# Kernel tuning notes

Hardware: AMD Instinct MI355X
Metric: run time of the kernel (lower is better)

Reference implementation:

```python
import jax, jax.numpy as jnp
import numpy as np

N, E, F_IN, F_OUT = 16384, 4096, 128, 128
EPS = 1e-6


def setup_inputs() -> dict:
    key = jax.random.key(0)
    k1, k2, k3 = jax.random.split(key, 3)
    H = (jax.random.uniform(k1, (N, E)) < 0.05).astype(jnp.float32)
    x = jax.random.normal(k2, (N, F_IN), dtype=jnp.float32)
    W = jax.random.normal(k3, (F_IN, F_OUT), dtype=jnp.float32) * 0.05
    return {"x": x, "H": H, "W": W}


def reference(x, H, W):
    # D_v^{-1} H D_e^{-1} H^T x W, computed without materializing the NxN
    # adjacency: diagonal matmuls become row/col broadcast scaling, and the
    # GEMM chain is reordered right-to-left (same math, associativity).
    d_e_inv = 1.0 / (H.sum(axis=0) + EPS)   # [E]
    d_v_inv = 1.0 / (H.sum(axis=1) + EPS)   # [N]
    xw = x @ W                               # [N, F_out]
    edge_msg = H.T @ xw                      # [E, F_out] gather onto edges
    edge_msg = d_e_inv[:, None] * edge_msg   # D_e^{-1}
    node_msg = H @ edge_msg                  # [N, F_out] scatter back to nodes
    return d_v_inv[:, None] * node_msg       # D_v^{-1}
```

## Files before the change

kernel.cpp:

```cpp
#include <hip/hip_runtime.h>
#include <stdint.h>

#define N_NODES 16384
#define N_EDGES 4096
#define FDIM    128
#define EPSF    1e-6f

typedef __attribute__((ext_vector_type(8))) short short8;
typedef __attribute__((ext_vector_type(4))) float f32x4;
typedef unsigned long long ull;

__device__ __forceinline__ unsigned short f2bf(float f) {
    uint32_t u = __float_as_uint(f);
    return (unsigned short)((u + 0x7FFFu + ((u >> 16) & 1u)) >> 16);
}
__device__ __forceinline__ short8 as_s8(uint4 v) {
    union { uint4 a; short8 b; } u; u.a = v; return u.b;
}

__device__ __forceinline__ short8 expand8(uint32_t half, int bitoff) {
    uint32_t b8 = (half >> bitoff) & 0xFFu;
    uint32_t lo = ((b8 & 0xFu) * 0x00204081u) & 0x01010101u;
    uint32_t hi = ((b8 >> 4) * 0x00204081u) & 0x01010101u;
    union { short8 v; uint32_t u[4]; } a;
#if __has_builtin(__builtin_amdgcn_perm)
    a.u[0] = __builtin_amdgcn_perm(0u, lo, 0x04010400u) * 0x3F80u;
    a.u[1] = __builtin_amdgcn_perm(0u, lo, 0x04030402u) * 0x3F80u;
    a.u[2] = __builtin_amdgcn_perm(0u, hi, 0x04010400u) * 0x3F80u;
    a.u[3] = __builtin_amdgcn_perm(0u, hi, 0x04030402u) * 0x3F80u;
#else
    a.u[0] = ((lo & 1u)         | ((lo >> 8) & 1u) << 16) * 0x3F80u;
    a.u[1] = (((lo >> 16) & 1u) | ((lo >> 24) & 1u) << 16) * 0x3F80u;
    a.u[2] = ((hi & 1u)         | ((hi >> 8) & 1u) << 16) * 0x3F80u;
    a.u[3] = (((hi >> 16) & 1u) | ((hi >> 24) & 1u) << 16) * 0x3F80u;
#endif
    return a.v;
}

__device__ __forceinline__ ull bit_transpose64(ull q, int lane) {
    const ull M32 = 0xFFFFFFFF00000000ull, M16 = 0xFFFF0000FFFF0000ull,
              M8 = 0xFF00FF00FF00FF00ull, M4 = 0xF0F0F0F0F0F0F0F0ull,
              M2 = 0xCCCCCCCCCCCCCCCCull, M1 = 0xAAAAAAAAAAAAAAAAull;
#define TSTEP(d, Md) { ull tv = __shfl_xor(q, d, 64); \
    q = ((lane & d) == 0) ? ((q & ~Md) | ((tv << d) & Md)) \
                          : ((q & Md) | ((tv >> d) & ~Md)); }
    TSTEP(32, M32) TSTEP(16, M16) TSTEP(8, M8) TSTEP(4, M4) TSTEP(2, M2) TSTEP(1, M1)
#undef TSTEP
    return q;
}

__global__ __launch_bounds__(256) void k_bitpack(const float* __restrict__ H,
        ull* __restrict__ bitsNE, float* __restrict__ dvinv) {
    int w = threadIdx.x >> 6, lane = threadIdx.x & 63;
    int n = blockIdx.x * 4 + w;
    const float4* hr = (const float4*)(H + (size_t)n * N_EDGES);
    ull* out = bitsNE + (size_t)n * (N_EDGES / 64);
    int cnt = 0;
    for (int c4 = 0; c4 < N_EDGES / 256; ++c4) {
        float4 v = hr[c4 * 64 + lane];
        ull b0 = __ballot(v.x > 0.5f);
        ull b1 = __ballot(v.y > 0.5f);
        ull b2 = __ballot(v.z > 0.5f);
        ull b3 = __ballot(v.w > 0.5f);
        cnt += __popcll(b0) + __popcll(b1) + __popcll(b2) + __popcll(b3);
        if (lane == 0) {
            #pragma unroll
            for (int q = 0; q < 4; ++q) {
                ull wq = ((b0 >> (16 * q)) & 0xFFFFull)
                       | (((b1 >> (16 * q)) & 0xFFFFull) << 16)
                       | (((b2 >> (16 * q)) & 0xFFFFull) << 32)
                       | (((b3 >> (16 * q)) & 0xFFFFull) << 48);
                out[c4 * 4 + q] = wq;
            }
        }
    }
    if (lane == 0) dvinv[n] = 1.0f / ((float)cnt + EPSF);
}

__global__ __launch_bounds__(256) void k_transpose_bf(const ull* __restrict__ bitsNE,
        ull* __restrict__ bitsEN) {
    int w = threadIdx.x >> 6, lane = threadIdx.x & 63;
    int wid = blockIdx.x * 4 + w;
    int nt = wid >> 3, etg = wid & 7;
    int pl = 4 * (lane & 15) + (lane >> 4);
    const ull* src = bitsNE + (size_t)(nt * 64 + pl) * (N_EDGES / 64);
    #pragma unroll
    for (int i = 0; i < 8; ++i) {
        int et = etg * 8 + i;
        ull q = src[et];
        q = bit_transpose64(q, lane);
        bitsEN[(size_t)(et * 64 + pl) * (N_NODES / 64) + nt] = q;
    }
}

__global__ __launch_bounds__(256) void k_edeg(const ull* __restrict__ bitsEN,
        float* __restrict__ deinv) {
    int w = threadIdx.x >> 6, lane = threadIdx.x & 63;
    int e = blockIdx.x * 4 + w;
    const ull* r = bitsEN + (size_t)e * (N_NODES / 64);
    int s = __popcll(r[lane]) + __popcll(r[lane + 64]) + __popcll(r[lane + 128]) + __popcll(r[lane + 192]);
    for (int o = 32; o; o >>= 1) s += __shfl_xor(s, o);
    if (lane == 0) deinv[e] = 1.0f / ((float)s + EPSF);
}

__global__ __launch_bounds__(256) void k_xw(const float* __restrict__ x, const float* __restrict__ W,
        unsigned short* __restrict__ xwTp) {
    __shared__ __attribute__((aligned(16))) unsigned short ldsWT[128 * 136];
    __shared__ __attribute__((aligned(16))) unsigned short ldsT[128 * 72];
    int t = threadIdx.x, lane = t & 63, w = t >> 6;
    int r16 = lane & 15, klane = lane >> 4;
    for (int i = 0; i < 64; ++i) {
        int idx = i * 256 + t;
        int k = idx >> 7, f = idx & 127;
        ldsWT[f * 136 + k] = f2bf(W[idx]);
    }
    __syncthreads();
    int nbase = blockIdx.x * 64;
    int row = nbase + w * 16 + r16;
    const float4* xr4 = (const float4*)(x + (size_t)row * FDIM);
    f32x4 acc[8] = {};
    for (int kb = 0; kb < 128; kb += 32) {
        float4 u0 = xr4[(kb >> 2) + klane * 2];
        float4 u1 = xr4[(kb >> 2) + klane * 2 + 1];
        union { short8 v; unsigned short u[8]; } a;
        a.u[0] = f2bf(u0.x); a.u[1] = f2bf(u0.y); a.u[2] = f2bf(u0.z); a.u[3] = f2bf(u0.w);
        a.u[4] = f2bf(u1.x); a.u[5] = f2bf(u1.y); a.u[6] = f2bf(u1.z); a.u[7] = f2bf(u1.w);
        #pragma unroll
        for (int fb = 0; fb < 8; ++fb) {
            short8 b = *(const short8*)&ldsWT[(fb * 16 + r16) * 136 + kb + klane * 8];
            acc[fb] = __builtin_amdgcn_mfma_f32_16x16x32_bf16(a.v, b, acc[fb], 0, 0, 0);
        }
    }
    #pragma unroll
    for (int fb = 0; fb < 8; ++fb)
        #pragma unroll
        for (int r = 0; r < 4; ++r)
            ldsT[(fb * 16 + r16) * 72 + 16 * r + w * 4 + klane] = f2bf(acc[fb][r]);
    __syncthreads();
    int f = t >> 1, part = t & 1;
    #pragma unroll
    for (int j = 0; j < 4; ++j)
        *(uint4*)&xwTp[(size_t)f * N_NODES + nbase + part * 32 + j * 8] =
            *(const uint4*)&ldsT[f * 72 + part * 32 + j * 8];
}

#define LOADP(Q0, Q1, BUF, p) do { \
    Q0 = brow0[(p)]; Q1 = brow1[(p)]; \
    const unsigned short* _src = bcol + (size_t)(p) * 64; \
    _Pragma("unroll") \
    for (int _fb = 0; _fb < 4; ++_fb) { \
        BUF[_fb * 2]     = *(const uint4*)(_src + _fb * fbstride); \
        BUF[_fb * 2 + 1] = *(const uint4*)(_src + _fb * fbstride + 32); \
    } } while (0)

#define COMPUTEP(Q0, Q1, BUF) do { \
    _Pragma("unroll") \
    for (int _s2 = 0; _s2 < 2; ++_s2) { \
        uint32_t _h0 = (uint32_t)(_s2 == 0 ? (Q0) : ((Q0) >> 32)); \
        uint32_t _h1 = (uint32_t)(_s2 == 0 ? (Q1) : ((Q1) >> 32)); \
        short8 _a0 = expand8(_h0, bitoff); \
        short8 _a1 = expand8(_h1, bitoff); \
        _Pragma("unroll") \
        for (int _f = 0; _f < 4; ++_f) { \
            short8 _b = as_s8(BUF[_f * 2 + _s2]); \
            acc[0][_f] = __builtin_amdgcn_mfma_f32_16x16x32_bf16(_a0, _b, acc[0][_f], 0, 0, 0); \
            acc[1][_f] = __builtin_amdgcn_mfma_f32_16x16x32_bf16(_a1, _b, acc[1][_f], 0, 0, 0); \
        } } } while (0)

template<bool FINAL>
__global__ __launch_bounds__(256, 2) void k_gemm_gen(
        const ull* __restrict__ bits, int krows,
        const unsigned short* __restrict__ BT, int K,
        float* __restrict__ Cout, const float* __restrict__ rowScale,
        int M, int npairs) {
    int t = threadIdx.x, lane = t & 63, w = t >> 6;
    int r16 = lane & 15, klane = lane >> 4;
    int bitoff = klane * 8;
    int wm = w >> 1, wf = w & 1;
    int mbase = blockIdx.x * 64 + wm * 32;
    int kq0 = blockIdx.z * npairs;
    const ull* brow0 = bits + (size_t)(mbase + r16) * krows + kq0;
    const ull* brow1 = brow0 + (size_t)16 * krows;
    const unsigned short* bcol = BT + (size_t)(wf * 64 + r16) * K + (size_t)kq0 * 64 + klane * 8;
    const size_t fbstride = (size_t)16 * K;
    f32x4 acc[2][4] = {};
    ull qA0, qA1, qB0, qB1;
    uint4 bufA[8], bufB[8];
    LOADP(qA0, qA1, bufA, 0);
    for (int p = 0; p < npairs; p += 2) {
        LOADP(qB0, qB1, bufB, p + 1);
        COMPUTEP(qA0, qA1, bufA);
        if (p + 2 < npairs) LOADP(qA0, qA1, bufA, p + 2);
        COMPUTEP(qB0, qB1, bufB);
    }
    #pragma unroll
    for (int fr = 0; fr < 2; ++fr)
        #pragma unroll
        for (int fb = 0; fb < 4; ++fb)
            #pragma unroll
            for (int r = 0; r < 4; ++r) {
                int row = mbase + fr * 16 + klane * 4 + r;
                int col = wf * 64 + fb * 16 + r16;
                float v = acc[fr][fb][r];
                if (FINAL)
                    Cout[(size_t)row * FDIM + col] = rowScale[row] * v;
                else
                    Cout[(size_t)blockIdx.z * M * FDIM + (size_t)row * FDIM + col] = v;
            }
}

__global__ __launch_bounds__(256) void k_reduce_scale_T(const float* __restrict__ partials,
        const float* __restrict__ deinv, unsigned short* __restrict__ emTp, int S) {
    __shared__ float lds[64 * 129];
    int t = threadIdx.x;
    int e0 = blockIdx.x * 64;
    for (int i = 0; i < 32; ++i) {
        int idx = i * 256 + t;
        int e_l = idx >> 7, f = idx & 127;
        float s = 0.f;
        for (int z = 0; z < S; ++z)
            s += partials[(size_t)z * N_EDGES * FDIM + (size_t)(e0 + e_l) * FDIM + f];
        lds[e_l * 129 + f] = s * deinv[e0 + e_l];
    }
    __syncthreads();
    for (int i = 0; i < 32; ++i) {
        int idx = i * 256 + t;
        int f = idx >> 6, j = idx & 63;
        int pj = 4 * (j & 15) + (j >> 4);
        emTp[(size_t)f * N_EDGES + e0 + j] = f2bf(lds[pj * 129 + f]);
    }
}

__global__ __launch_bounds__(256) void k_finalN(const float* __restrict__ partN,
        const float* __restrict__ dvinv, float* __restrict__ out) {
    const float4* pa = (const float4*)partN;
    const float4* pb = (const float4*)(partN + (size_t)N_NODES * FDIM);
    float4* o4 = (float4*)out;
    int t = threadIdx.x;
    #pragma unroll
    for (int i = 0; i < 4; ++i) {
        int idx = blockIdx.x * 1024 + i * 256 + t;
        float4 a = pa[idx], b = pb[idx];
        float s = dvinv[idx >> 5];
        o4[idx] = make_float4((a.x + b.x) * s, (a.y + b.y) * s,
                              (a.z + b.z) * s, (a.w + b.w) * s);
    }
}

extern "C" void kernel_launch(void* const* d_in, const int* in_sizes, int n_in,
                              void* d_out, int out_size, void* d_ws, size_t ws_size,
                              hipStream_t stream) {
    const float* x = (const float*)d_in[0];
    const float* H = (const float*)d_in[1];
    const float* W = (const float*)d_in[2];
    float* out = (float*)d_out;
    char* ws = (char*)d_ws;

    ull* bitsNE = (ull*)(ws);
    ull* bitsEN = (ull*)(ws + (8u << 20));
    unsigned short* xwTp = (unsigned short*)(ws + (16u << 20));
    unsigned short* emTp = (unsigned short*)(ws + (20u << 20));
    float* dvinv = (float*)(ws + (21u << 20));
    float* deinv = (float*)(ws + (21u << 20) + 65536);
    float* partE = (float*)(ws + (22u << 20));
    float* partN = (float*)(ws + (38u << 20));

    int SE = 8;
    while (SE > 1 && (22u << 20) + (size_t)SE * N_EDGES * FDIM * 4 > ws_size) SE >>= 1;
    bool sn2 = ws_size >= ((38u << 20) + (size_t)2 * N_NODES * FDIM * 4);

    hipLaunchKernelGGL(k_bitpack, dim3(4096), dim3(256), 0, stream, H, bitsNE, dvinv);
    hipLaunchKernelGGL(k_transpose_bf, dim3(512), dim3(256), 0, stream, bitsNE, bitsEN);
    hipLaunchKernelGGL(k_edeg, dim3(1024), dim3(256), 0, stream, bitsEN, deinv);
    hipLaunchKernelGGL(k_xw, dim3(256), dim3(256), 0, stream, x, W, xwTp);
    hipLaunchKernelGGL((k_gemm_gen<false>), dim3(64, 1, SE), dim3(256), 0, stream,
                       bitsEN, N_NODES / 64, xwTp, N_NODES, partE, (const float*)nullptr,
                       N_EDGES, (N_NODES / 64) / SE);
    hipLaunchKernelGGL(k_reduce_scale_T, dim3(64), dim3(256), 0, stream, partE, deinv, emTp, SE);
    if (sn2) {
        hipLaunchKernelGGL((k_gemm_gen<false>), dim3(256, 1, 2), dim3(256), 0, stream,
                           bitsNE, N_EDGES / 64, emTp, N_EDGES, partN, (const float*)nullptr,
                           N_NODES, (N_EDGES / 64) / 2);
        hipLaunchKernelGGL(k_finalN, dim3(512), dim3(256), 0, stream, partN, dvinv, out);
    } else {
        hipLaunchKernelGGL((k_gemm_gen<true>), dim3(256, 1, 1), dim3(256), 0, stream,
                           bitsNE, N_EDGES / 64, emTp, N_EDGES, out, dvinv,
                           N_NODES, N_EDGES / 64);
    }
}
```

Baseline: 302.2 us.

## Fuse edge-degree count into transpose, repack bits per lane, drop split-K node GEMM

Bitpacking now has each lane read 64 contiguous floats and build one 64-bit word from exponent bits, replacing the per-wave ballot loop. The lane permutation used in the bit layout is removed. The separate edge-degree kernel is dropped: degrees are accumulated with atomics inside the transpose kernel, and the reciprocal is computed in the reduce kernel. The node-side GEMM goes from a 2-way split plus finalize kernel to a single launch that scales rows in its epilogue. The 2-blocks-per-CU launch bound on the GEMM is relaxed. Together these cut launches and intermediate traffic, at the cost of atomics and less parallelism in the final GEMM.

```diff
diff --git a/kernel.cpp b/kernel.cpp
--- a/kernel.cpp
+++ b/kernel.cpp
@@ -50,61 +50,61 @@
 }
 
 __global__ __launch_bounds__(256) void k_bitpack(const float* __restrict__ H,
-        ull* __restrict__ bitsNE, float* __restrict__ dvinv) {
-    int w = threadIdx.x >> 6, lane = threadIdx.x & 63;
-    int n = blockIdx.x * 4 + w;
-    const float4* hr = (const float4*)(H + (size_t)n * N_EDGES);
-    ull* out = bitsNE + (size_t)n * (N_EDGES / 64);
-    int cnt = 0;
-    for (int c4 = 0; c4 < N_EDGES / 256; ++c4) {
-        float4 v = hr[c4 * 64 + lane];
-        ull b0 = __ballot(v.x > 0.5f);
-        ull b1 = __ballot(v.y > 0.5f);
-        ull b2 = __ballot(v.z > 0.5f);
-        ull b3 = __ballot(v.w > 0.5f);
-        cnt += __popcll(b0) + __popcll(b1) + __popcll(b2) + __popcll(b3);
-        if (lane == 0) {
-            #pragma unroll
-            for (int q = 0; q < 4; ++q) {
-                ull wq = ((b0 >> (16 * q)) & 0xFFFFull)
-                       | (((b1 >> (16 * q)) & 0xFFFFull) << 16)
-                       | (((b2 >> (16 * q)) & 0xFFFFull) << 32)
-                       | (((b3 >> (16 * q)) & 0xFFFFull) << 48);
-                out[c4 * 4 + q] = wq;
-            }
+        ull* __restrict__ bitsNE, float* __restrict__ dvinv, int* __restrict__ ecnt) {
+    int t = threadIdx.x, w = t >> 6, lane = t & 63;
+    if (blockIdx.x == 0) {
+        int4 z = make_int4(0, 0, 0, 0);
+        #pragma unroll
+        for (int i = 0; i < 4; ++i) ((int4*)ecnt)[t * 4 + i] = z;
+    }
+    #pragma unroll
+    for (int r2 = 0; r2 < 2; ++r2) {
+        int n = blockIdx.x * 8 + w * 2 + r2;
+        const uint4* hr = (const uint4*)(H + (size_t)n * N_EDGES) + lane * 16;
+        uint32_t lo = 0, hi = 0;
+        #pragma unroll
+        for (int j = 0; j < 8; ++j) {
+            uint4 u = hr[j];
+            lo |= ((u.x >> 23) & 1u) << (4 * j);
+            lo |= ((u.y >> 23) & 1u) << (4 * j + 1);
+            lo |= ((u.z >> 23) & 1u) << (4 * j + 2);
+            lo |= ((u.w >> 23) & 1u) << (4 * j + 3);
         }
-    }
-    if (lane == 0) dvinv[n] = 1.0f / ((float)cnt + EPSF);
+        #pragma unroll
+        for (int j = 0; j < 8; ++j) {
+            uint4 u = hr[8 + j];
+            hi |= ((u.x >> 23) & 1u) << (4 * j);
+            hi |= ((u.y >> 23) & 1u) << (4 * j + 1);
+            hi |= ((u.z >> 23) & 1u) << (4 * j + 2);
+            hi |= ((u.w >> 23) & 1u) << (4 * j + 3);
+        }
+        ull q = (ull)lo | ((ull)hi << 32);
+        bitsNE[(size_t)n * (N_EDGES / 64) + lane] = q;
+        int cnt = __popcll(q);
+        #pragma unroll
+        for (int o = 32; o; o >>= 1) cnt += __shfl_xor(cnt, o);
+        if (lane == 0) dvinv[n] = 1.0f / ((float)cnt + EPSF);
+    }
 }
 
 __global__ __launch_bounds__(256) void k_transpose_bf(const ull* __restrict__ bitsNE,
-        ull* __restrict__ bitsEN) {
+        ull* __restrict__ bitsEN, int* __restrict__ ecnt) {
     int w = threadIdx.x >> 6, lane = threadIdx.x & 63;
     int wid = blockIdx.x * 4 + w;
     int nt = wid >> 3, etg = wid & 7;
-    int pl = 4 * (lane & 15) + (lane >> 4);
-    const ull* src = bitsNE + (size_t)(nt * 64 + pl) * (N_EDGES / 64);
+    const ull* src = bitsNE + (size_t)(nt * 64 + lane) * (N_EDGES / 64);
     #pragma unroll
     for (int i = 0; i < 8; ++i) {
         int et = etg * 8 + i;
         ull q = src[et];
         q = bit_transpose64(q, lane);
-        bitsEN[(size_t)(et * 64 + pl) * (N_NODES / 64) + nt] = q;
-    }
-}
-
-__global__ __launch_bounds__(256) void k_edeg(const ull* __restrict__ bitsEN,
-        float* __restrict__ deinv) {
-    int w = threadIdx.x >> 6, lane = threadIdx.x & 63;
-    int e = blockIdx.x * 4 + w;
-    const ull* r = bitsEN + (size_t)e * (N_NODES / 64);
-    int s = __popcll(r[lane]) + __popcll(r[lane + 64]) + __popcll(r[lane + 128]) + __popcll(r[lane + 192]);
-    for (int o = 32; o; o >>= 1) s += __shfl_xor(s, o);
-    if (lane == 0) deinv[e] = 1.0f / ((float)s + EPSF);
+        bitsEN[(size_t)(et * 64 + lane) * (N_NODES / 64) + nt] = q;
+        atomicAdd(&ecnt[et * 64 + lane], __popcll(q));
+    }
 }
 
 __global__ __launch_bounds__(256) void k_xw(const float* __restrict__ x, const float* __restrict__ W,
-        unsigned short* __restrict__ xwTp) {
+        unsigned short* __restrict__ xwT) {
     __shared__ __attribute__((aligned(16))) unsigned short ldsWT[128 * 136];
     __shared__ __attribute__((aligned(16))) unsigned short ldsT[128 * 72];
     int t = threadIdx.x, lane = t & 63, w = t >> 6;
@@ -135,12 +135,12 @@
     for (int fb = 0; fb < 8; ++fb)
         #pragma unroll
         for (int r = 0; r < 4; ++r)
-            ldsT[(fb * 16 + r16) * 72 + 16 * r + w * 4 + klane] = f2bf(acc[fb][r]);
+            ldsT[(fb * 16 + r16) * 72 + w * 16 + klane * 4 + r] = f2bf(acc[fb][r]);
     __syncthreads();
     int f = t >> 1, part = t & 1;
     #pragma unroll
     for (int j = 0; j < 4; ++j)
-        *(uint4*)&xwTp[(size_t)f * N_NODES + nbase + part * 32 + j * 8] =
+        *(uint4*)&xwT[(size_t)f * N_NODES + nbase + part * 32 + j * 8] =
             *(const uint4*)&ldsT[f * 72 + part * 32 + j * 8];
 }
 
@@ -168,7 +168,7 @@
         } } } while (0)
 
 template<bool FINAL>
-__global__ __launch_bounds__(256, 2) void k_gemm_gen(
+__global__ __launch_bounds__(256) void k_gemm_gen(
         const ull* __restrict__ bits, int krows,
         const unsigned short* __restrict__ BT, int K,
         float* __restrict__ Cout, const float* __restrict__ rowScale,
@@ -210,40 +210,25 @@
 }
 
 __global__ __launch_bounds__(256) void k_reduce_scale_T(const float* __restrict__ partials,
-        const float* __restrict__ deinv, unsigned short* __restrict__ emTp, int S) {
+        const int* __restrict__ ecnt, unsigned short* __restrict__ emT, int S) {
     __shared__ float lds[64 * 129];
+    __shared__ float sdeinv[64];
     int t = threadIdx.x;
     int e0 = blockIdx.x * 64;
+    if (t < 64) sdeinv[t] = 1.0f / ((float)ecnt[e0 + t] + EPSF);
     for (int i = 0; i < 32; ++i) {
         int idx = i * 256 + t;
         int e_l = idx >> 7, f = idx & 127;
         float s = 0.f;
         for (int z = 0; z < S; ++z)
             s += partials[(size_t)z * N_EDGES * FDIM + (size_t)(e0 + e_l) * FDIM + f];
-        lds[e_l * 129 + f] = s * deinv[e0 + e_l];
+        lds[e_l * 129 + f] = s;
     }
     __syncthreads();
     for (int i = 0; i < 32; ++i) {
         int idx = i * 256 + t;
         int f = idx >> 6, j = idx & 63;
-        int pj = 4 * (j & 15) + (j >> 4);
-        emTp[(size_t)f * N_EDGES + e0 + j] = f2bf(lds[pj * 129 + f]);
-    }
-}
-
-__global__ __launch_bounds__(256) void k_finalN(const float* __restrict__ partN,
-        const float* __restrict__ dvinv, float* __restrict__ out) {
-    const float4* pa = (const float4*)partN;
-    const float4* pb = (const float4*)(partN + (size_t)N_NODES * FDIM);
-    float4* o4 = (float4*)out;
-    int t = threadIdx.x;
-    #pragma unroll
-    for (int i = 0; i < 4; ++i) {
-        int idx = blockIdx.x * 1024 + i * 256 + t;
-        float4 a = pa[idx], b = pb[idx];
-        float s = dvinv[idx >> 5];
-        o4[idx] = make_float4((a.x + b.x) * s, (a.y + b.y) * s,
-                              (a.z + b.z) * s, (a.w + b.w) * s);
+        emT[(size_t)f * N_EDGES + e0 + j] = f2bf(lds[j * 129 + f] * sdeinv[j]);
     }
 }
 
@@ -258,33 +243,23 @@
 
     ull* bitsNE = (ull*)(ws);
     ull* bitsEN = (ull*)(ws + (8u << 20));
-    unsigned short* xwTp = (unsigned short*)(ws + (16u << 20));
-    unsigned short* emTp = (unsigned short*)(ws + (20u << 20));
+    unsigned short* xwT = (unsigned short*)(ws + (16u << 20));
+    unsigned short* emT = (unsigned short*)(ws + (20u << 20));
     float* dvinv = (float*)(ws + (21u << 20));
-    float* deinv = (float*)(ws + (21u << 20) + 65536);
+    int* ecnt = (int*)(ws + (21u << 20) + 65536);
     float* partE = (float*)(ws + (22u << 20));
-    float* partN = (float*)(ws + (38u << 20));
 
     int SE = 8;
     while (SE > 1 && (22u << 20) + (size_t)SE * N_EDGES * FDIM * 4 > ws_size) SE >>= 1;
-    bool sn2 = ws_size >= ((38u << 20) + (size_t)2 * N_NODES * FDIM * 4);
-
-    hipLaunchKernelGGL(k_bitpack, dim3(4096), dim3(256), 0, stream, H, bitsNE, dvinv);
-    hipLaunchKernelGGL(k_transpose_bf, dim3(512), dim3(256), 0, stream, bitsNE, bitsEN);
-    hipLaunchKernelGGL(k_edeg, dim3(1024), dim3(256), 0, stream, bitsEN, deinv);
-    hipLaunchKernelGGL(k_xw, dim3(256), dim3(256), 0, stream, x, W, xwTp);
+
+    hipLaunchKernelGGL(k_bitpack, dim3(2048), dim3(256), 0, stream, H, bitsNE, dvinv, ecnt);
+    hipLaunchKernelGGL(k_transpose_bf, dim3(512), dim3(256), 0, stream, bitsNE, bitsEN, ecnt);
+    hipLaunchKernelGGL(k_xw, dim3(256), dim3(256), 0, stream, x, W, xwT);
     hipLaunchKernelGGL((k_gemm_gen<false>), dim3(64, 1, SE), dim3(256), 0, stream,
-                       bitsEN, N_NODES / 64, xwTp, N_NODES, partE, (const float*)nullptr,
+                       bitsEN, N_NODES / 64, xwT, N_NODES, partE, (const float*)nullptr,
                        N_EDGES, (N_NODES / 64) / SE);
-    hipLaunchKernelGGL(k_reduce_scale_T, dim3(64), dim3(256), 0, stream, partE, deinv, emTp, SE);
-    if (sn2) {
-        hipLaunchKernelGGL((k_gemm_gen<false>), dim3(256, 1, 2), dim3(256), 0, stream,
-                           bitsNE, N_EDGES / 64, emTp, N_EDGES, partN, (const float*)nullptr,
-                           N_NODES, (N_EDGES / 64) / 2);
-        hipLaunchKernelGGL(k_finalN, dim3(512), dim3(256), 0, stream, partN, dvinv, out);
-    } else {
-        hipLaunchKernelGGL((k_gemm_gen<true>), dim3(256, 1, 1), dim3(256), 0, stream,
-                           bitsNE, N_EDGES / 64, emTp, N_EDGES, out, dvinv,
-                           N_NODES, N_EDGES / 64);
-    }
-}
+    hipLaunchKernelGGL(k_reduce_scale_T, dim3(64), dim3(256), 0, stream, partE, ecnt, emT, SE);
+    hipLaunchKernelGGL((k_gemm_gen<true>), dim3(256, 1, 1), dim3(256), 0, stream,
+                       bitsNE, N_EDGES / 64, emT, N_EDGES, out, dvinv,
+                       N_NODES, N_EDGES / 64);
+}
```

Result: slower. 314.3 us (+4.0%).
